# Kernel tuning notes

Hardware: AMD Instinct MI355X
Metric: run time of the kernel (lower is better)

## Reference

```python
import jax, jax.numpy as jnp
import numpy as np

N_NODES = 100000
K_STEPS = 10
ALPHA = 0.1


def setup_inputs() -> dict:
    key = jax.random.key(0)
    k1, k2, k3, k4 = jax.random.split(key, 4)
    x = jax.random.normal(k1, (N_NODES, 512), dtype=jnp.float32)
    edge_index = jax.random.randint(k2, (2, 3200000), 0, N_NODES, dtype=jnp.int64)
    W1 = jax.random.normal(k3, (512, 256), dtype=jnp.float32) * (1.0 / np.sqrt(512))
    b1 = jnp.zeros((256,), dtype=jnp.float32)
    W2 = jax.random.normal(k4, (256, 64), dtype=jnp.float32) * (1.0 / np.sqrt(256))
    b2 = jnp.zeros((64,), dtype=jnp.float32)
    return {"x": x, "edge_index": edge_index, "W1": W1, "b1": b1, "W2": W2, "b2": b2}


def _gcn_norm(edge_index, num_nodes):
    # Add self loops and compute symmetric normalization deg^-1/2 A deg^-1/2.
    loops = jnp.arange(num_nodes, dtype=edge_index.dtype)
    src = jnp.concatenate([edge_index[0], loops])
    dst = jnp.concatenate([edge_index[1], loops])
    deg = jax.ops.segment_sum(jnp.ones_like(dst, dtype=jnp.float32), dst,
                              num_segments=num_nodes)
    dinv = jnp.where(deg > 0, jax.lax.rsqrt(deg), 0.0)
    norm = dinv[src] * dinv[dst]  # [E + N]
    return src, dst, norm


def reference(x, edge_index, W1, b1, W2, b2):
    n = x.shape[0]
    # MLP (dropout is identity at inference)
    h = jax.nn.relu(x @ W1 + b1)
    h = h @ W2 + b2  # [N, C]
    # APPNP propagation: h_{k+1} = (1-alpha) * A_hat h_k + alpha * h_0
    src, dst, norm = _gcn_norm(edge_index, n)
    h0 = h

    def step(carry, _):
        msg = carry[src] * norm[:, None]                     # gather + scale
        agg = jax.ops.segment_sum(msg, dst, num_segments=n)  # scatter-add
        return (1.0 - ALPHA) * agg + ALPHA * h0, None

    h, _ = jax.lax.scan(step, h, None, length=K_STEPS)
    return jax.nn.log_softmax(h, axis=1)
```

## Files before the change

### kernel.cpp

```cpp
#include <hip/hip_runtime.h>
#include <cstdint>
#include <cstddef>


typedef _Float16 half8 __attribute__((ext_vector_type(8)));
typedef float floatx4 __attribute__((ext_vector_type(4)));

__device__ inline float2 unpack2(uint u) {
    union { uint u; _Float16 h[2]; } c; c.u = u;
    return make_float2((float)c.h[0], (float)c.h[1]);
}
__device__ inline uint pack2(float a, float b) {
    union { uint u; _Float16 h[2]; } c; c.h[0] = (_Float16)a; c.h[1] = (_Float16)b;
    return c.u;
}

__global__ void transpose_w1_tiled(const float* __restrict__ W1, _Float16* __restrict__ W1tt) {
    int i = blockIdx.x * 256 + threadIdx.x;
    if (i < 512 * 256) {
        int kt = i >> 13, c = (i >> 5) & 255, j = i & 31;
        W1tt[i] = (_Float16)W1[(size_t)(kt * 32 + j) * 256 + c];
    }
}
__global__ void transpose_w2(const float* __restrict__ W2, _Float16* __restrict__ W2t) {
    int i = blockIdx.x * 256 + threadIdx.x;
    if (i < 256 * 64) {
        int k = i >> 6, c = i & 63;
        W2t[(size_t)c * 256 + k] = (_Float16)W2[i];
    }
}

__global__ __launch_bounds__(256) void mlp_kernel(
    const float* __restrict__ x, const _Float16* __restrict__ W1tt,
    const float* __restrict__ b1, const _Float16* __restrict__ W2t,
    const float* __restrict__ b2, const float* __restrict__ dinv,
    _Float16* __restrict__ g0h, int n)
{
    __shared__ __align__(16) _Float16 xs[32][520];
    __shared__ __align__(16) _Float16 wraw[2][10240];

    const int tid  = threadIdx.x;
    const int lane = tid & 63;
    const int wid  = tid >> 6;
    const int r0blk = blockIdx.x * 32;
    const int lr = lane & 15;
    const int lg = lane >> 4;

    for (int fi = tid; fi < 32 * 128; fi += 256) {
        int r = fi >> 7, k4 = (fi & 127) * 4;
        float4 v = *(const float4*)(x + (size_t)(r0blk + r) * 512 + k4);
        union { short4 s; _Float16 h[4]; } c;
        c.h[0] = (_Float16)v.x; c.h[1] = (_Float16)v.y;
        c.h[2] = (_Float16)v.z; c.h[3] = (_Float16)v.w;
        *(short4*)&xs[r][k4] = c.s;
    }

    const int wr = wid >> 1, wc = wid & 1;
    floatx4 acc1[8];
#pragma unroll
    for (int ct = 0; ct < 8; ++ct) {
        float b = b1[wc * 128 + ct * 16 + lr];
        acc1[ct] = (floatx4){b, b, b, b};
    }

    const int sc = tid >> 2, ss = (tid & 3) * 8;
    int4 st0, st1, st2, st3;
    {
        const int4* gs = (const int4*)(W1tt);
        st0 = gs[tid]; st1 = gs[tid + 256]; st2 = gs[tid + 512]; st3 = gs[tid + 768];
    }
    {
        _Float16* wb = wraw[0];
        *(int4*)&wb[(sc +   0) * 40 + ss] = st0;
        *(int4*)&wb[(sc +  64) * 40 + ss] = st1;
        *(int4*)&wb[(sc + 128) * 40 + ss] = st2;
        *(int4*)&wb[(sc + 192) * 40 + ss] = st3;
    }
    __syncthreads();

    for (int kt = 0; kt < 16; ++kt) {
        const int cur = kt & 1;
        if (kt < 15) {
            const int4* gs = (const int4*)(W1tt + (size_t)(kt + 1) * 8192);
            st0 = gs[tid]; st1 = gs[tid + 256]; st2 = gs[tid + 512]; st3 = gs[tid + 768];
        }
        const _Float16* wb = wraw[cur];
        half8 a = *(const half8*)&xs[wr * 16 + lr][kt * 32 + lg * 8];
#pragma unroll
        for (int ct = 0; ct < 8; ++ct) {
            half8 b = *(const half8*)&wb[(wc * 128 + ct * 16 + lr) * 40 + lg * 8];
            acc1[ct] = __builtin_amdgcn_mfma_f32_16x16x32_f16(a, b, acc1[ct], 0, 0, 0);
        }
        if (kt < 15) {
            _Float16* wn = wraw[cur ^ 1];
            *(int4*)&wn[(sc +   0) * 40 + ss] = st0;
            *(int4*)&wn[(sc +  64) * 40 + ss] = st1;
            *(int4*)&wn[(sc + 128) * 40 + ss] = st2;
            *(int4*)&wn[(sc + 192) * 40 + ss] = st3;
        }
        __syncthreads();
    }

    _Float16 (*hmid)[264] = (_Float16(*)[264])&wraw[0][0];
#pragma unroll
    for (int ct = 0; ct < 8; ++ct) {
#pragma unroll
        for (int r = 0; r < 4; ++r) {
            float v = fmaxf(acc1[ct][r], 0.f);
            hmid[wr * 16 + lg * 4 + r][wc * 128 + ct * 16 + lr] = (_Float16)v;
        }
    }
    __syncthreads();

    const int rt = wid >> 1, ct2 = (wid & 1) * 2;
    floatx4 acc2[2] = {(floatx4){0,0,0,0}, (floatx4){0,0,0,0}};
#pragma unroll 2
    for (int kk = 0; kk < 256; kk += 32) {
        half8 a = *(const half8*)&hmid[rt * 16 + lr][kk + lg * 8];
#pragma unroll
        for (int q = 0; q < 2; ++q) {
            half8 b = *(const half8*)&W2t[(size_t)((ct2 + q) * 16 + lr) * 256 + kk + lg * 8];
            acc2[q] = __builtin_amdgcn_mfma_f32_16x16x32_f16(a, b, acc2[q], 0, 0, 0);
        }
    }
#pragma unroll
    for (int q = 0; q < 2; ++q) {
        int col = (ct2 + q) * 16 + lr;
        float bb = b2[col];
#pragma unroll
        for (int r = 0; r < 4; ++r) {
            int row = r0blk + rt * 16 + lg * 4 + r;
            float di = dinv[row];
            g0h[(size_t)row * 64 + col] = (_Float16)(di * (acc2[q][r] + bb));
        }
    }
}

__global__ void init_counts_kernel(int* __restrict__ counts, int n) {
    int i = blockIdx.x * blockDim.x + threadIdx.x;
    if (i < n) counts[i] = 1;
}

__global__ void count_kernel(const int* __restrict__ dstL, int* __restrict__ counts,
                             int e, int rs, int n) {
    const int r = blockIdx.x & 7;
    const int g = blockIdx.x >> 3;
    const int B = gridDim.x >> 3;
    const int lo = r * rs;
    const int hi = min(lo + rs, n);
    for (int i = g * blockDim.x + threadIdx.x; i < e; i += B * blockDim.x) {
        int d = dstL[i];
        if (d >= lo && d < hi) atomicAdd(&counts[d], 1);
    }
}

__global__ void dinv_kernel(const int* __restrict__ counts, float* __restrict__ dinv,
                            float* __restrict__ Anode, int n) {
    int i = blockIdx.x * blockDim.x + threadIdx.x;
    if (i < n) {
        float deg = (float)counts[i];
        dinv[i] = 1.0f / sqrtf(deg);
        Anode[i] = 0.9f / deg;
    }
}

__global__ __launch_bounds__(256) void scan_a(const int* __restrict__ counts,
                                              int* __restrict__ rowptr,
                                              int* __restrict__ bsums, int n)
{
    __shared__ int s[256];
    const int t = threadIdx.x;
    const int i = blockIdx.x * 256 + t;
    int v = (i < n) ? (counts[i] - 1) : 0;
    s[t] = v;
    __syncthreads();
    for (int off = 1; off < 256; off <<= 1) {
        int add = (t >= off) ? s[t - off] : 0;
        __syncthreads();
        s[t] += add;
        __syncthreads();
    }
    if (i < n) rowptr[i] = s[t] - v;
    if (t == 255) bsums[blockIdx.x] = s[255];
}

__global__ __launch_bounds__(512) void scan_b(const int* __restrict__ bsums,
                                              int* __restrict__ boff, int nb)
{
    __shared__ int s[512];
    const int t = threadIdx.x;
    int v = (t < nb) ? bsums[t] : 0;
    s[t] = v;
    __syncthreads();
    for (int off = 1; off < 512; off <<= 1) {
        int add = (t >= off) ? s[t - off] : 0;
        __syncthreads();
        s[t] += add;
        __syncthreads();
    }
    if (t < nb) boff[t] = s[t] - v;
}

__global__ __launch_bounds__(256) void scan_c(int* __restrict__ rowptr,
                                              int* __restrict__ cursor,
                                              const int* __restrict__ boff, int n, int e)
{
    int i = blockIdx.x * 256 + threadIdx.x;
    if (i < n) {
        int v = rowptr[i] + boff[blockIdx.x];
        rowptr[i] = v;
        cursor[i] = v;
    }
    if (i == 0) rowptr[n] = e;
}

__global__ void fill_kernel(const int* __restrict__ srcL, const int* __restrict__ dstL,
                            int* __restrict__ cursor, int* __restrict__ srcs,
                            int e, int rs, int n) {
    const int r = blockIdx.x & 7;
    const int g = blockIdx.x >> 3;
    const int B = gridDim.x >> 3;
    const int lo = r * rs;
    const int hi = min(lo + rs, n);
    for (int i = g * blockDim.x + threadIdx.x; i < e; i += B * blockDim.x) {
        int d = dstL[i];
        if (d >= lo && d < hi) {
            int pos = atomicAdd(&cursor[d], 1);
            srcs[pos] = srcL[i];
        }
    }
}

__global__ __launch_bounds__(256) void prop_kernel(
    const uint* __restrict__ gu, const uint* __restrict__ g0u,
    uint* __restrict__ gnu, const int* __restrict__ rowptr,
    const int* __restrict__ srcs, const float* __restrict__ Anode, int n)
{
    const int node = (blockIdx.x * blockDim.x + threadIdx.x) >> 6;
    if (node >= n) return;
    const int lane = threadIdx.x & 63;
    const int half_ = lane >> 5;
    const int p = lane & 31;
    const int e0 = rowptr[node], e1 = rowptr[node + 1];
    float accx = 0.f, accy = 0.f;
    int e = e0 + half_;
    for (; e + 6 < e1; e += 8) {
        int s0 = srcs[e], s1 = srcs[e + 2], s2 = srcs[e + 4], s3 = srcs[e + 6];
        float2 f0 = unpack2(gu[(size_t)s0 * 32 + p]);
        float2 f1 = unpack2(gu[(size_t)s1 * 32 + p]);
        float2 f2 = unpack2(gu[(size_t)s2 * 32 + p]);
        float2 f3 = unpack2(gu[(size_t)s3 * 32 + p]);
        accx += f0.x; accy += f0.y;
        accx += f1.x; accy += f1.y;
        accx += f2.x; accy += f2.y;
        accx += f3.x; accy += f3.y;
    }
    for (; e < e1; e += 2) {
        float2 f = unpack2(gu[(size_t)srcs[e] * 32 + p]);
        accx += f.x; accy += f.y;
    }
    accx += __shfl_xor(accx, 32);
    accy += __shfl_xor(accy, 32);

    const float A = Anode[node];
    float2 self = unpack2(gu[(size_t)node * 32 + p]);
    float2 anc  = unpack2(g0u[(size_t)node * 32 + p]);
    float ox = A * (accx + self.x) + 0.1f * anc.x;
    float oy = A * (accy + self.y) + 0.1f * anc.y;
    if (half_ == 0) gnu[(size_t)node * 32 + p] = pack2(ox, oy);
}

__global__ __launch_bounds__(256) void logsoftmax_kernel(
    const _Float16* __restrict__ g, const float* __restrict__ dinv,
    float* __restrict__ out, int n)
{
    const int row = (blockIdx.x * blockDim.x + threadIdx.x) >> 6;
    const int lane = threadIdx.x & 63;
    if (row >= n) return;
    float v = (float)g[(size_t)row * 64 + lane] / dinv[row];
    float m = v;
#pragma unroll
    for (int o = 32; o > 0; o >>= 1) m = fmaxf(m, __shfl_xor(m, o));
    float ex = expf(v - m);
    float s = ex;
#pragma unroll
    for (int o = 32; o > 0; o >>= 1) s += __shfl_xor(s, o);
    out[(size_t)row * 64 + lane] = v - m - logf(s);
}

extern "C" void kernel_launch(void* const* d_in, const int* in_sizes, int n_in,
                              void* d_out, int out_size, void* d_ws, size_t ws_size,
                              hipStream_t stream)
{
    const float* x  = (const float*)d_in[0];
    const int*   ei = (const int*)d_in[1];
    const float* W1 = (const float*)d_in[2];
    const float* b1 = (const float*)d_in[3];
    const float* W2 = (const float*)d_in[4];
    const float* b2 = (const float*)d_in[5];
    float* out = (float*)d_out;

    const int n = in_sizes[0] / 512;
    const int e = in_sizes[1] / 2;
    const int* srcL = ei;
    const int* dstL = ei + e;

    char* wsb = (char*)d_ws;
    size_t off = 0;
    auto alloc = [&](size_t bytes) -> void* {
        void* p = wsb + off;
        off = (off + bytes + 255) & ~(size_t)255;
        return p;
    };
    _Float16* g0h = (_Float16*)alloc((size_t)n * 64 * 2);
    _Float16* gp0 = (_Float16*)alloc((size_t)n * 64 * 2);
    _Float16* gp1 = (_Float16*)alloc((size_t)n * 64 * 2);
    int*   srcs   = (int*)alloc((size_t)e * 4);
    float* dinv   = (float*)alloc((size_t)n * 4);
    float* Anode  = (float*)alloc((size_t)n * 4);
    int*   counts = (int*)alloc((size_t)n * 4);
    int*   rowptr = (int*)alloc((size_t)(n + 1) * 4);
    int*   bsums  = (int*)alloc(4096);
    int*   boff   = (int*)alloc(4096);
    _Float16* W1tt = (_Float16*)alloc((size_t)512 * 256 * 2);
    _Float16* W2t  = (_Float16*)alloc((size_t)256 * 64 * 2);
    int* cursor = counts;

    const int nb = (n + 255) / 256;
    const int rs = (n + 7) / 8;

    transpose_w1_tiled<<<(512 * 256 + 255) / 256, 256, 0, stream>>>(W1, W1tt);
    transpose_w2<<<(256 * 64 + 255) / 256, 256, 0, stream>>>(W2, W2t);

    init_counts_kernel<<<nb, 256, 0, stream>>>(counts, n);
    count_kernel<<<1024, 256, 0, stream>>>(dstL, counts, e, rs, n);
    dinv_kernel<<<nb, 256, 0, stream>>>(counts, dinv, Anode, n);
    scan_a<<<nb, 256, 0, stream>>>(counts, rowptr, bsums, n);
    scan_b<<<1, 512, 0, stream>>>(bsums, boff, nb);
    scan_c<<<nb, 256, 0, stream>>>(rowptr, cursor, boff, n, e);
    fill_kernel<<<1024, 256, 0, stream>>>(srcL, dstL, cursor, srcs, e, rs, n);

    mlp_kernel<<<n / 32, 256, 0, stream>>>(x, W1tt, b1, W2t, b2, dinv, g0h, n);

    const int pgrid = (n * 64 + 255) / 256;
    const uint* gin = (const uint*)g0h;
    uint* bufs[2] = {(uint*)gp0, (uint*)gp1};
    for (int it = 0; it < 10; ++it) {
        uint* gn = bufs[it & 1];
        prop_kernel<<<pgrid, 256, 0, stream>>>(gin, (const uint*)g0h, gn,
                                               rowptr, srcs, Anode, n);
        gin = gn;
    }
    logsoftmax_kernel<<<pgrid, 256, 0, stream>>>((const _Float16*)gin, dinv, out, n);
}
```

Baseline: 1.445 ms.

## Load MLP weights directly from fragment-tiled global layout; deepen gather unroll

The first MLP layer no longer stages W1 through double-buffered shared memory with a barrier every k-step. Instead each wave reads its MFMA B-fragments straight from a new fragment-major global layout, which is likely L2-resident, and covers two row tiles so each fragment is reused twice. W2 gets the same fragment layout, which makes its reads contiguous. The propagation gather loop also unrolls from 4 to 8 independent loads per iteration for more memory-level parallelism. The cost is more global or L2 traffic for the weights per block and higher register pressure.

```diff
diff --git a/kernel.cpp b/kernel.cpp
--- a/kernel.cpp
+++ b/kernel.cpp
@@ -15,29 +15,29 @@
     return c.u;
 }
 
-__global__ void transpose_w1_tiled(const float* __restrict__ W1, _Float16* __restrict__ W1tt) {
+__global__ void transpose_w1c(const float* __restrict__ W1, _Float16* __restrict__ W1tc) {
     int i = blockIdx.x * 256 + threadIdx.x;
     if (i < 512 * 256) {
-        int kt = i >> 13, c = (i >> 5) & 255, j = i & 31;
-        W1tt[i] = (_Float16)W1[(size_t)(kt * 32 + j) * 256 + c];
-    }
-}
-__global__ void transpose_w2(const float* __restrict__ W2, _Float16* __restrict__ W2t) {
+        int kt = i >> 13, ctile = (i >> 9) & 15, col = (i >> 5) & 15, j = i & 31;
+        W1tc[i] = (_Float16)W1[(size_t)(kt * 32 + j) * 256 + ctile * 16 + col];
+    }
+}
+__global__ void transpose_w2c(const float* __restrict__ W2, _Float16* __restrict__ W2tc) {
     int i = blockIdx.x * 256 + threadIdx.x;
     if (i < 256 * 64) {
-        int k = i >> 6, c = i & 63;
-        W2t[(size_t)c * 256 + k] = (_Float16)W2[i];
+        int kt = i >> 11, ct = (i >> 9) & 3, col = (i >> 5) & 15, j = i & 31;
+        W2tc[i] = (_Float16)W2[(size_t)(kt * 32 + j) * 64 + ct * 16 + col];
     }
 }
 
 __global__ __launch_bounds__(256) void mlp_kernel(
-    const float* __restrict__ x, const _Float16* __restrict__ W1tt,
-    const float* __restrict__ b1, const _Float16* __restrict__ W2t,
+    const float* __restrict__ x, const _Float16* __restrict__ W1tc,
+    const float* __restrict__ b1, const _Float16* __restrict__ W2tc,
     const float* __restrict__ b2, const float* __restrict__ dinv,
     _Float16* __restrict__ g0h, int n)
 {
     __shared__ __align__(16) _Float16 xs[32][520];
-    __shared__ __align__(16) _Float16 wraw[2][10240];
+    __shared__ __align__(16) _Float16 hmid[32][264];
 
     const int tid  = threadIdx.x;
     const int lane = tid & 63;
@@ -54,72 +54,50 @@
         c.h[2] = (_Float16)v.z; c.h[3] = (_Float16)v.w;
         *(short4*)&xs[r][k4] = c.s;
     }
-
-    const int wr = wid >> 1, wc = wid & 1;
-    floatx4 acc1[8];
-#pragma unroll
-    for (int ct = 0; ct < 8; ++ct) {
-        float b = b1[wc * 128 + ct * 16 + lr];
-        acc1[ct] = (floatx4){b, b, b, b};
-    }
-
-    const int sc = tid >> 2, ss = (tid & 3) * 8;
-    int4 st0, st1, st2, st3;
-    {
-        const int4* gs = (const int4*)(W1tt);
-        st0 = gs[tid]; st1 = gs[tid + 256]; st2 = gs[tid + 512]; st3 = gs[tid + 768];
-    }
-    {
-        _Float16* wb = wraw[0];
-        *(int4*)&wb[(sc +   0) * 40 + ss] = st0;
-        *(int4*)&wb[(sc +  64) * 40 + ss] = st1;
-        *(int4*)&wb[(sc + 128) * 40 + ss] = st2;
-        *(int4*)&wb[(sc + 192) * 40 + ss] = st3;
-    }
     __syncthreads();
 
+    floatx4 acc1[2][4];
+#pragma unroll
+    for (int c = 0; c < 4; ++c) {
+        float b = b1[wid * 64 + c * 16 + lr];
+        acc1[0][c] = (floatx4){b, b, b, b};
+        acc1[1][c] = (floatx4){b, b, b, b};
+    }
+
+#pragma unroll 2
     for (int kt = 0; kt < 16; ++kt) {
-        const int cur = kt & 1;
-        if (kt < 15) {
-            const int4* gs = (const int4*)(W1tt + (size_t)(kt + 1) * 8192);
-            st0 = gs[tid]; st1 = gs[tid + 256]; st2 = gs[tid + 512]; st3 = gs[tid + 768];
+        half8 bf[4];
+#pragma unroll
+        for (int c = 0; c < 4; ++c)
+            bf[c] = *(const half8*)&W1tc[(((size_t)kt * 16 + wid * 4 + c) * 16 + lr) * 32 + lg * 8];
+        half8 a0 = *(const half8*)&xs[lr][kt * 32 + lg * 8];
+        half8 a1 = *(const half8*)&xs[16 + lr][kt * 32 + lg * 8];
+#pragma unroll
+        for (int c = 0; c < 4; ++c) {
+            acc1[0][c] = __builtin_amdgcn_mfma_f32_16x16x32_f16(a0, bf[c], acc1[0][c], 0, 0, 0);
+            acc1[1][c] = __builtin_amdgcn_mfma_f32_16x16x32_f16(a1, bf[c], acc1[1][c], 0, 0, 0);
         }
-        const _Float16* wb = wraw[cur];
-        half8 a = *(const half8*)&xs[wr * 16 + lr][kt * 32 + lg * 8];
-#pragma unroll
-        for (int ct = 0; ct < 8; ++ct) {
-            half8 b = *(const half8*)&wb[(wc * 128 + ct * 16 + lr) * 40 + lg * 8];
-            acc1[ct] = __builtin_amdgcn_mfma_f32_16x16x32_f16(a, b, acc1[ct], 0, 0, 0);
-        }
-        if (kt < 15) {
-            _Float16* wn = wraw[cur ^ 1];
-            *(int4*)&wn[(sc +   0) * 40 + ss] = st0;
-            *(int4*)&wn[(sc +  64) * 40 + ss] = st1;
-            *(int4*)&wn[(sc + 128) * 40 + ss] = st2;
-            *(int4*)&wn[(sc + 192) * 40 + ss] = st3;
-        }
-        __syncthreads();
-    }
-
-    _Float16 (*hmid)[264] = (_Float16(*)[264])&wraw[0][0];
-#pragma unroll
-    for (int ct = 0; ct < 8; ++ct) {
-#pragma unroll
-        for (int r = 0; r < 4; ++r) {
-            float v = fmaxf(acc1[ct][r], 0.f);
-            hmid[wr * 16 + lg * 4 + r][wc * 128 + ct * 16 + lr] = (_Float16)v;
-        }
-    }
+    }
+
+#pragma unroll
+    for (int rt = 0; rt < 2; ++rt)
+#pragma unroll
+        for (int c = 0; c < 4; ++c)
+#pragma unroll
+            for (int r = 0; r < 4; ++r) {
+                float v = fmaxf(acc1[rt][c][r], 0.f);
+                hmid[rt * 16 + lg * 4 + r][wid * 64 + c * 16 + lr] = (_Float16)v;
+            }
     __syncthreads();
 
     const int rt = wid >> 1, ct2 = (wid & 1) * 2;
     floatx4 acc2[2] = {(floatx4){0,0,0,0}, (floatx4){0,0,0,0}};
-#pragma unroll 2
-    for (int kk = 0; kk < 256; kk += 32) {
-        half8 a = *(const half8*)&hmid[rt * 16 + lr][kk + lg * 8];
+#pragma unroll
+    for (int kt = 0; kt < 8; ++kt) {
+        half8 a = *(const half8*)&hmid[rt * 16 + lr][kt * 32 + lg * 8];
 #pragma unroll
         for (int q = 0; q < 2; ++q) {
-            half8 b = *(const half8*)&W2t[(size_t)((ct2 + q) * 16 + lr) * 256 + kk + lg * 8];
+            half8 b = *(const half8*)&W2tc[((size_t)(kt * 4 + ct2 + q) * 16 + lr) * 32 + lg * 8];
             acc2[q] = __builtin_amdgcn_mfma_f32_16x16x32_f16(a, b, acc2[q], 0, 0, 0);
         }
     }
@@ -244,16 +222,25 @@
     const int e0 = rowptr[node], e1 = rowptr[node + 1];
     float accx = 0.f, accy = 0.f;
     int e = e0 + half_;
-    for (; e + 6 < e1; e += 8) {
-        int s0 = srcs[e], s1 = srcs[e + 2], s2 = srcs[e + 4], s3 = srcs[e + 6];
+    for (; e + 14 < e1; e += 16) {
+        int s0 = srcs[e],      s1 = srcs[e + 2],  s2 = srcs[e + 4],  s3 = srcs[e + 6];
+        int s4 = srcs[e + 8],  s5 = srcs[e + 10], s6 = srcs[e + 12], s7 = srcs[e + 14];
         float2 f0 = unpack2(gu[(size_t)s0 * 32 + p]);
         float2 f1 = unpack2(gu[(size_t)s1 * 32 + p]);
         float2 f2 = unpack2(gu[(size_t)s2 * 32 + p]);
         float2 f3 = unpack2(gu[(size_t)s3 * 32 + p]);
+        float2 f4 = unpack2(gu[(size_t)s4 * 32 + p]);
+        float2 f5 = unpack2(gu[(size_t)s5 * 32 + p]);
+        float2 f6 = unpack2(gu[(size_t)s6 * 32 + p]);
+        float2 f7 = unpack2(gu[(size_t)s7 * 32 + p]);
         accx += f0.x; accy += f0.y;
         accx += f1.x; accy += f1.y;
         accx += f2.x; accy += f2.y;
         accx += f3.x; accy += f3.y;
+        accx += f4.x; accy += f4.y;
+        accx += f5.x; accy += f5.y;
+        accx += f6.x; accy += f6.y;
+        accx += f7.x; accy += f7.y;
     }
     for (; e < e1; e += 2) {
         float2 f = unpack2(gu[(size_t)srcs[e] * 32 + p]);
@@ -322,15 +309,15 @@
     int*   rowptr = (int*)alloc((size_t)(n + 1) * 4);
     int*   bsums  = (int*)alloc(4096);
     int*   boff   = (int*)alloc(4096);
-    _Float16* W1tt = (_Float16*)alloc((size_t)512 * 256 * 2);
-    _Float16* W2t  = (_Float16*)alloc((size_t)256 * 64 * 2);
+    _Float16* W1tc = (_Float16*)alloc((size_t)512 * 256 * 2);
+    _Float16* W2tc = (_Float16*)alloc((size_t)256 * 64 * 2);
     int* cursor = counts;
 
     const int nb = (n + 255) / 256;
     const int rs = (n + 7) / 8;
 
-    transpose_w1_tiled<<<(512 * 256 + 255) / 256, 256, 0, stream>>>(W1, W1tt);
-    transpose_w2<<<(256 * 64 + 255) / 256, 256, 0, stream>>>(W2, W2t);
+    transpose_w1c<<<(512 * 256 + 255) / 256, 256, 0, stream>>>(W1, W1tc);
+    transpose_w2c<<<(256 * 64 + 255) / 256, 256, 0, stream>>>(W2, W2tc);
 
     init_counts_kernel<<<nb, 256, 0, stream>>>(counts, n);
     count_kernel<<<1024, 256, 0, stream>>>(dstL, counts, e, rs, n);
@@ -340,7 +327,7 @@
     scan_c<<<nb, 256, 0, stream>>>(rowptr, cursor, boff, n, e);
     fill_kernel<<<1024, 256, 0, stream>>>(srcL, dstL, cursor, srcs, e, rs, n);
 
-    mlp_kernel<<<n / 32, 256, 0, stream>>>(x, W1tt, b1, W2t, b2, dinv, g0h, n);
+    mlp_kernel<<<n / 32, 256, 0, stream>>>(x, W1tc, b1, W2tc, b2, dinv, g0h, n);
 
     const int pgrid = (n * 64 + 255) / 256;
     const uint* gin = (const uint*)g0h;
```

Result: no change. 1.435 ms (-0.7%).
